# Kernel optimization log

Hardware: AMD Instinct MI355X
Metric: run time of the kernel (lower is better)

The kernel has to match this reference:

```python
import jax, jax.numpy as jnp
import numpy as np

N = 2_000_000      # active input voxels
C = 32             # channels
GRID = 128         # spatial grid extent per axis
B = 8              # batch size
KERNEL = 2
STRIDE = 2
PAD = 0
MODE = "avg"       # 'avg' or 'max'


def setup_inputs() -> dict:
    key = jax.random.key(0)
    k1, k2, k3 = jax.random.split(key, 3)
    b = jax.random.randint(k1, (N, 1), 0, B, dtype=jnp.int32)
    xyz = jax.random.randint(k2, (N, 3), 0, GRID, dtype=jnp.int32)
    coords = jnp.concatenate([b, xyz], axis=1)          # [N,4] = (batch, x, y, z)
    feats = jax.random.normal(k3, (N, C), dtype=jnp.float32)
    return {"feats": feats, "coords": coords}


def reference(feats, coords):
    # Downsampled coordinate of the output cell each input voxel falls into
    # (non-overlapping pooling: kernel_size == stride).
    out_grid = (GRID + 2 * PAD + STRIDE - 1) // STRIDE   # 64
    oc = (coords[:, 1:] + PAD) // STRIDE                 # [N,3] int32
    # Linearized hash key: (batch, ox, oy, oz) -> scalar
    key = ((coords[:, 0] * out_grid + oc[:, 0]) * out_grid + oc[:, 1]) * out_grid + oc[:, 2]
    # jit-compatible unique with static size = N (upper bound on #output voxels);
    # padded slots get fill_value=-1 and zero count.
    uniq_keys, inv = jnp.unique(key, size=N, fill_value=-1, return_inverse=True)
    if MODE == "avg":
        sums = jax.ops.segment_sum(feats, inv, num_segments=N)            # [N,C]
        cnt = jax.ops.segment_sum(jnp.ones((N,), feats.dtype), inv, num_segments=N)
        out_feats = sums / jnp.maximum(cnt, 1.0)[:, None]
    else:
        out_feats = jax.ops.segment_max(feats, inv, num_segments=N)       # [N,C]
    # out_feats: pooled features per unique output voxel (padded rows are zeros/-inf)
    return out_feats, uniq_keys
```

## Files before the change

kernel.cpp:

```cpp
#include <hip/hip_runtime.h>
#include <stdint.h>


#define KS (1u << 21)
#define KMASK (KS - 1u)
#define SCAN_BLOCKS 1024
#define SCAN_TPB 256
#define EPT 8
#define C 32

typedef float vf4 __attribute__((ext_vector_type(4)));

__global__ void k_zero(uint4* __restrict__ p, int n4) {
  int i = blockIdx.x * blockDim.x + threadIdx.x;
  if (i < n4) p[i] = make_uint4(0u, 0u, 0u, 0u);
}

__global__ void k_count(const int4* __restrict__ coords, uint32_t* __restrict__ keys,
                        uint32_t* __restrict__ cnt, int n) {
  int i = blockIdx.x * blockDim.x + threadIdx.x;
  if (i >= n) return;
  int4 cc = coords[i];
  uint32_t k = (((uint32_t)cc.x * 64u + ((uint32_t)cc.y >> 1)) * 64u
                + ((uint32_t)cc.z >> 1)) * 64u + ((uint32_t)cc.w >> 1);
  uint32_t r = atomicAdd(&cnt[k], 1u);
  keys[i] = k | (r << 21);
}

__global__ void k_blocksum(const uint32_t* __restrict__ cnt,
                           uint32_t* __restrict__ blkP, uint32_t* __restrict__ blkM) {
  __shared__ uint32_t sp[SCAN_TPB], sm[SCAN_TPB];
  int t = threadIdx.x;
  int base = blockIdx.x * (SCAN_TPB * EPT) + t * EPT;
  const uint4* c4 = (const uint4*)(cnt + base);
  uint4 q0 = c4[0], q1 = c4[1];
  uint32_t p = (q0.x > 0) + (q0.y > 0) + (q0.z > 0) + (q0.w > 0)
             + (q1.x > 0) + (q1.y > 0) + (q1.z > 0) + (q1.w > 0);
  uint32_t m = q0.x + q0.y + q0.z + q0.w + q1.x + q1.y + q1.z + q1.w;
  sp[t] = p; sm[t] = m;
  __syncthreads();
  for (int off = SCAN_TPB / 2; off > 0; off >>= 1) {
    if (t < off) { sp[t] += sp[t + off]; sm[t] += sm[t + off]; }
    __syncthreads();
  }
  if (t == 0) { blkP[blockIdx.x] = sp[0]; blkM[blockIdx.x] = sm[0]; }
}

__global__ void k_scan_blksums(uint32_t* __restrict__ blkP, uint32_t* __restrict__ blkM,
                               uint32_t* __restrict__ totalK) {
  __shared__ uint32_t sp[SCAN_BLOCKS], sm[SCAN_BLOCKS];
  int t = threadIdx.x;
  sp[t] = blkP[t]; sm[t] = blkM[t];
  __syncthreads();
  for (int off = 1; off < SCAN_BLOCKS; off <<= 1) {
    uint32_t vp = (t >= off) ? sp[t - off] : 0u;
    uint32_t vm = (t >= off) ? sm[t - off] : 0u;
    __syncthreads();
    sp[t] += vp; sm[t] += vm;
    __syncthreads();
  }
  blkP[t] = t ? sp[t - 1] : 0u;
  blkM[t] = t ? sm[t - 1] : 0u;
  if (t == SCAN_BLOCKS - 1) *totalK = sp[SCAN_BLOCKS - 1];
}

__global__ void k_finalize(const uint32_t* __restrict__ cnt,
                           const uint32_t* __restrict__ blkP, const uint32_t* __restrict__ blkM,
                           uint32_t* __restrict__ cur,
                           uint64_t* __restrict__ denseMeta,
                           float* __restrict__ uniqOut) {
  __shared__ uint32_t sp[SCAN_TPB], sm[SCAN_TPB];
  int t = threadIdx.x;
  int base = blockIdx.x * (SCAN_TPB * EPT) + t * EPT;
  const uint4* c4 = (const uint4*)(cnt + base);
  uint4 q0 = c4[0], q1 = c4[1];
  uint32_t c[EPT] = {q0.x, q0.y, q0.z, q0.w, q1.x, q1.y, q1.z, q1.w};
  uint32_t p = 0, m = 0;
#pragma unroll
  for (int e = 0; e < EPT; e++) { p += (c[e] > 0); m += c[e]; }
  sp[t] = p; sm[t] = m;
  __syncthreads();
  for (int off = 1; off < SCAN_TPB; off <<= 1) {
    uint32_t vp = (t >= off) ? sp[t - off] : 0u;
    uint32_t vm = (t >= off) ? sm[t - off] : 0u;
    __syncthreads();
    sp[t] += vp; sm[t] += vm;
    __syncthreads();
  }
  uint32_t poff = blkP[blockIdx.x] + (t ? sp[t - 1] : 0u);
  uint32_t moff = blkM[blockIdx.x] + (t ? sm[t - 1] : 0u);
#pragma unroll
  for (int e = 0; e < EPT; e++) {
    if (c[e] > 0) {
      uint32_t k = (uint32_t)base + (uint32_t)e;
      cur[k] = moff;
      denseMeta[poff] = ((uint64_t)c[e] << 32) | (uint64_t)moff;
      uniqOut[poff]   = (float)k;
      poff++;
    }
    moff += c[e];
  }
}

__global__ void k_scatter(const uint32_t* __restrict__ keys, const uint32_t* __restrict__ cur,
                          uint32_t* __restrict__ sortedIdx, int n) {
  int i = blockIdx.x * blockDim.x + threadIdx.x;
  if (i >= n) return;
  uint32_t kk = keys[i];
  uint32_t pos = cur[kk & KMASK] + (kk >> 21);
  sortedIdx[pos] = (uint32_t)i;
}

__global__ __launch_bounds__(256, 8)
void k_pool(const float* __restrict__ feats, const uint32_t* __restrict__ sortedIdx,
            const uint64_t* __restrict__ denseMeta, const uint32_t* __restrict__ totalK,
            float* __restrict__ outFeats, float* __restrict__ uniqOut, int n) {
  const int tid = threadIdx.x;
  const int hw = tid >> 5;
  const int lane = tid & 31;
  const int subrow = lane >> 3;
  const int cl = lane & 7;
  const uint32_t K = *totalK;
  const int j0 = (blockIdx.x * 8 + hw) * 8;
  const int jA = j0 + subrow;
  const int jB = j0 + 4 + subrow;

  const bool vA = jA < n, vB = jB < n;
  const bool lA = vA && (uint32_t)jA < K;
  const bool lB = vB && (uint32_t)jB < K;

  uint32_t sA = 0, cA = 0, sB = 0, cB = 0;
  if (lA) { uint64_t dm = denseMeta[jA]; sA = (uint32_t)dm; cA = (uint32_t)(dm >> 32); }
  if (lB) { uint64_t dm = denseMeta[jB]; sB = (uint32_t)dm; cB = (uint32_t)(dm >> 32); }

  uint32_t iA = 0, iB = 0;
  if (lA && (uint32_t)cl < cA) iA = sortedIdx[sA + (uint32_t)cl];
  if (lB && (uint32_t)cl < cB) iB = sortedIdx[sB + (uint32_t)cl];

  vf4 aA = {0.f, 0.f, 0.f, 0.f}, aB = {0.f, 0.f, 0.f, 0.f};
#pragma unroll
  for (int q = 0; q < 4; ++q) {
    uint32_t uA = (uint32_t)__shfl((int)iA, (subrow << 3) | q, 32);
    uint32_t uB = (uint32_t)__shfl((int)iB, (subrow << 3) | q, 32);
    vf4 xA = *(const vf4*)(feats + (size_t)uA * C + cl * 4);
    vf4 xB = *(const vf4*)(feats + (size_t)uB * C + cl * 4);
    aA += ((uint32_t)q < cA) ? xA : (vf4){0.f, 0.f, 0.f, 0.f};
    aB += ((uint32_t)q < cB) ? xB : (vf4){0.f, 0.f, 0.f, 0.f};
  }
  for (uint32_t q = 4; q < 8u; ++q) {
    if (__all((int)(q >= cA && q >= cB))) break;
    uint32_t uA = (uint32_t)__shfl((int)iA, (int)(((uint32_t)subrow << 3) | q), 32);
    uint32_t uB = (uint32_t)__shfl((int)iB, (int)(((uint32_t)subrow << 3) | q), 32);
    if (q < cA) aA += *(const vf4*)(feats + (size_t)uA * C + cl * 4);
    if (q < cB) aB += *(const vf4*)(feats + (size_t)uB * C + cl * 4);
  }
  if (__any((int)(cA > 8u || cB > 8u))) {
    for (uint32_t q = 8; q < cA; ++q)
      aA += *(const vf4*)(feats + (size_t)sortedIdx[sA + q] * C + cl * 4);
    for (uint32_t q = 8; q < cB; ++q)
      aB += *(const vf4*)(feats + (size_t)sortedIdx[sB + q] * C + cl * 4);
  }

  if (vA) {
    float inv = lA ? 1.0f / (float)cA : 0.0f;
    vf4 o = aA * inv;
    __builtin_nontemporal_store(o, (vf4*)(outFeats + (size_t)jA * C + cl * 4));
    if (!lA && cl == 0) uniqOut[jA] = -1.0f;
  }
  if (vB) {
    float inv = lB ? 1.0f / (float)cB : 0.0f;
    vf4 o = aB * inv;
    __builtin_nontemporal_store(o, (vf4*)(outFeats + (size_t)jB * C + cl * 4));
    if (!lB && cl == 0) uniqOut[jB] = -1.0f;
  }
}

extern "C" void kernel_launch(void* const* d_in, const int* in_sizes, int n_in,
                              void* d_out, int out_size, void* d_ws, size_t ws_size,
                              hipStream_t stream) {
  const float* feats = (const float*)d_in[0];
  const int4* coords = (const int4*)d_in[1];
  int n = in_sizes[0] / C;

  char* ws = (char*)d_ws;
  const size_t MB = 1024u * 1024u;
  uint32_t* keys      = (uint32_t*)(ws + 0 * MB);
  uint32_t* cnt       = (uint32_t*)(ws + 8 * MB);
  uint32_t* cur       = (uint32_t*)(ws + 16 * MB);
  uint64_t* denseMeta = (uint64_t*)(ws + 24 * MB);
  uint32_t* sortedIdx = (uint32_t*)(ws + 40 * MB);
  uint32_t* blkP      = (uint32_t*)(ws + 48 * MB);
  uint32_t* blkM      = blkP + SCAN_BLOCKS;
  uint32_t* totalK    = blkM + SCAN_BLOCKS;

  float* outFeats = (float*)d_out;
  float* uniqOut  = outFeats + (size_t)n * C;

  k_zero<<<KS / 4 / 256, 256, 0, stream>>>((uint4*)cnt, KS / 4);
  k_count<<<(n + 255) / 256, 256, 0, stream>>>(coords, keys, cnt, n);
  k_blocksum<<<SCAN_BLOCKS, SCAN_TPB, 0, stream>>>(cnt, blkP, blkM);
  k_scan_blksums<<<1, SCAN_BLOCKS, 0, stream>>>(blkP, blkM, totalK);
  k_finalize<<<SCAN_BLOCKS, SCAN_TPB, 0, stream>>>(cnt, blkP, blkM, cur, denseMeta, uniqOut);
  k_scatter<<<(n + 255) / 256, 256, 0, stream>>>(keys, cur, sortedIdx, n);
  k_pool<<<(n + 63) / 64, 256, 0, stream>>>(feats, sortedIdx, denseMeta, totalK, outFeats, uniqOut, n);
}
```

Measured before the change: 260.5 us.

## Fold block-sum scan into finalize and unroll count/scatter kernels

Removes the single-block scan kernel. Each finalize block now reduces all 1024 block sums itself, packed as 64-bit (P,M) pairs, to get its own exclusive offset, and block 0 writes the total. This removes one launch and its serial dependency, at the cost of every block redundantly reading the 8KB of block sums. The count and scatter kernels now process 4 elements per thread, issuing loads ahead to raise memory-level parallelism.

```diff
diff --git a/kernel.cpp b/kernel.cpp
--- a/kernel.cpp
+++ b/kernel.cpp
@@ -8,6 +8,7 @@
 #define SCAN_TPB 256
 #define EPT 8
 #define C 32
+#define UNROLL 4
 
 typedef float vf4 __attribute__((ext_vector_type(4)));
 
@@ -18,13 +19,24 @@
 
 __global__ void k_count(const int4* __restrict__ coords, uint32_t* __restrict__ keys,
                         uint32_t* __restrict__ cnt, int n) {
-  int i = blockIdx.x * blockDim.x + threadIdx.x;
-  if (i >= n) return;
-  int4 cc = coords[i];
-  uint32_t k = (((uint32_t)cc.x * 64u + ((uint32_t)cc.y >> 1)) * 64u
-                + ((uint32_t)cc.z >> 1)) * 64u + ((uint32_t)cc.w >> 1);
-  uint32_t r = atomicAdd(&cnt[k], 1u);
-  keys[i] = k | (r << 21);
+  int base = blockIdx.x * (256 * UNROLL) + threadIdx.x;
+  int4 cc[UNROLL];
+  uint32_t k[UNROLL];
+#pragma unroll
+  for (int u = 0; u < UNROLL; ++u) {
+    int i = base + u * 256;
+    if (i < n) cc[u] = coords[i];
+  }
+#pragma unroll
+  for (int u = 0; u < UNROLL; ++u) {
+    int i = base + u * 256;
+    if (i < n) {
+      k[u] = (((uint32_t)cc[u].x * 64u + ((uint32_t)cc[u].y >> 1)) * 64u
+              + ((uint32_t)cc[u].z >> 1)) * 64u + ((uint32_t)cc[u].w >> 1);
+      uint32_t r = atomicAdd(&cnt[k[u]], 1u);
+      keys[i] = k[u] | (r << 21);
+    }
+  }
 }
 
 __global__ void k_blocksum(const uint32_t* __restrict__ cnt,
@@ -46,32 +58,34 @@
   if (t == 0) { blkP[blockIdx.x] = sp[0]; blkM[blockIdx.x] = sm[0]; }
 }
 
-__global__ void k_scan_blksums(uint32_t* __restrict__ blkP, uint32_t* __restrict__ blkM,
-                               uint32_t* __restrict__ totalK) {
-  __shared__ uint32_t sp[SCAN_BLOCKS], sm[SCAN_BLOCKS];
-  int t = threadIdx.x;
-  sp[t] = blkP[t]; sm[t] = blkM[t];
-  __syncthreads();
-  for (int off = 1; off < SCAN_BLOCKS; off <<= 1) {
-    uint32_t vp = (t >= off) ? sp[t - off] : 0u;
-    uint32_t vm = (t >= off) ? sm[t - off] : 0u;
-    __syncthreads();
-    sp[t] += vp; sm[t] += vm;
-    __syncthreads();
-  }
-  blkP[t] = t ? sp[t - 1] : 0u;
-  blkM[t] = t ? sm[t - 1] : 0u;
-  if (t == SCAN_BLOCKS - 1) *totalK = sp[SCAN_BLOCKS - 1];
-}
-
 __global__ void k_finalize(const uint32_t* __restrict__ cnt,
                            const uint32_t* __restrict__ blkP, const uint32_t* __restrict__ blkM,
                            uint32_t* __restrict__ cur,
                            uint64_t* __restrict__ denseMeta,
-                           float* __restrict__ uniqOut) {
+                           float* __restrict__ uniqOut,
+                           uint32_t* __restrict__ totalK) {
+  __shared__ uint64_t rAll[SCAN_TPB], rBel[SCAN_TPB];
   __shared__ uint32_t sp[SCAN_TPB], sm[SCAN_TPB];
-  int t = threadIdx.x;
-  int base = blockIdx.x * (SCAN_TPB * EPT) + t * EPT;
+  const int t = threadIdx.x;
+  const int b = blockIdx.x;
+
+  uint64_t all = 0, bel = 0;
+  for (int u = t; u < SCAN_BLOCKS; u += SCAN_TPB) {
+    uint64_t v = ((uint64_t)blkP[u] << 32) | (uint64_t)blkM[u];
+    all += v;
+    if (u < b) bel += v;
+  }
+  rAll[t] = all; rBel[t] = bel;
+  __syncthreads();
+  for (int off = SCAN_TPB / 2; off > 0; off >>= 1) {
+    if (t < off) { rAll[t] += rAll[t + off]; rBel[t] += rBel[t + off]; }
+    __syncthreads();
+  }
+  const uint32_t blockP = (uint32_t)(rBel[0] >> 32);
+  const uint32_t blockM = (uint32_t)rBel[0];
+  if (b == 0 && t == 0) *totalK = (uint32_t)(rAll[0] >> 32);
+
+  int base = b * (SCAN_TPB * EPT) + t * EPT;
   const uint4* c4 = (const uint4*)(cnt + base);
   uint4 q0 = c4[0], q1 = c4[1];
   uint32_t c[EPT] = {q0.x, q0.y, q0.z, q0.w, q1.x, q1.y, q1.z, q1.w};
@@ -87,8 +101,8 @@
     sp[t] += vp; sm[t] += vm;
     __syncthreads();
   }
-  uint32_t poff = blkP[blockIdx.x] + (t ? sp[t - 1] : 0u);
-  uint32_t moff = blkM[blockIdx.x] + (t ? sm[t - 1] : 0u);
+  uint32_t poff = blockP + (t ? sp[t - 1] : 0u);
+  uint32_t moff = blockM + (t ? sm[t - 1] : 0u);
 #pragma unroll
   for (int e = 0; e < EPT; e++) {
     if (c[e] > 0) {
@@ -104,11 +118,21 @@
 
 __global__ void k_scatter(const uint32_t* __restrict__ keys, const uint32_t* __restrict__ cur,
                           uint32_t* __restrict__ sortedIdx, int n) {
-  int i = blockIdx.x * blockDim.x + threadIdx.x;
-  if (i >= n) return;
-  uint32_t kk = keys[i];
-  uint32_t pos = cur[kk & KMASK] + (kk >> 21);
-  sortedIdx[pos] = (uint32_t)i;
+  int base = blockIdx.x * (256 * UNROLL) + threadIdx.x;
+  uint32_t kk[UNROLL];
+#pragma unroll
+  for (int u = 0; u < UNROLL; ++u) {
+    int i = base + u * 256;
+    if (i < n) kk[u] = keys[i];
+  }
+#pragma unroll
+  for (int u = 0; u < UNROLL; ++u) {
+    int i = base + u * 256;
+    if (i < n) {
+      uint32_t pos = cur[kk[u] & KMASK] + (kk[u] >> 21);
+      sortedIdx[pos] = (uint32_t)i;
+    }
+  }
 }
 
 __global__ __launch_bounds__(256, 8)
@@ -196,11 +220,11 @@
   float* outFeats = (float*)d_out;
   float* uniqOut  = outFeats + (size_t)n * C;
 
+  int chunk = 256 * UNROLL;
   k_zero<<<KS / 4 / 256, 256, 0, stream>>>((uint4*)cnt, KS / 4);
-  k_count<<<(n + 255) / 256, 256, 0, stream>>>(coords, keys, cnt, n);
+  k_count<<<(n + chunk - 1) / chunk, 256, 0, stream>>>(coords, keys, cnt, n);
   k_blocksum<<<SCAN_BLOCKS, SCAN_TPB, 0, stream>>>(cnt, blkP, blkM);
-  k_scan_blksums<<<1, SCAN_BLOCKS, 0, stream>>>(blkP, blkM, totalK);
-  k_finalize<<<SCAN_BLOCKS, SCAN_TPB, 0, stream>>>(cnt, blkP, blkM, cur, denseMeta, uniqOut);
-  k_scatter<<<(n + 255) / 256, 256, 0, stream>>>(keys, cur, sortedIdx, n);
+  k_finalize<<<SCAN_BLOCKS, SCAN_TPB, 0, stream>>>(cnt, blkP, blkM, cur, denseMeta, uniqOut, totalK);
+  k_scatter<<<(n + chunk - 1) / chunk, 256, 0, stream>>>(keys, cur, sortedIdx, n);
   k_pool<<<(n + 63) / 64, 256, 0, stream>>>(feats, sortedIdx, denseMeta, totalK, outFeats, uniqOut, n);
 }
```

Result: no change. 258.6 us (-0.7%).
